# Performance work log

Hardware: AMD Instinct MI355X
Metric: run time of the kernel (lower is better)

## Reference

```python
import jax, jax.numpy as jnp
import numpy as np

B, H, W, DIM = 16, 64, 64, 512
GH, GW = 8, 8
NH = 16
HD = DIM // NH
POS = DIM // 16  # DynamicPosBias pos_dim = (dim//4)//4 = 32
EPS = 1e-5


def setup_inputs() -> dict:
    key = jax.random.key(0)
    ks = jax.random.split(key, 12)
    w = lambda k, s: jax.random.normal(k, s, jnp.float32) * 0.02
    f32 = jnp.float32
    return {
        "x": jax.random.normal(ks[0], (B, H * W, DIM), f32),
        "norm1_g": jnp.ones((DIM,), f32), "norm1_b": jnp.zeros((DIM,), f32),
        "qkv_w": w(ks[1], (3 * DIM, DIM)), "qkv_b": jnp.zeros((3 * DIM,), f32),
        "proj_w": w(ks[2], (DIM, DIM)), "proj_b": jnp.zeros((DIM,), f32),
        "pos_w0": w(ks[3], (POS, 2)), "pos_b0": jnp.zeros((POS,), f32),
        "pos_ln0_g": jnp.ones((POS,), f32), "pos_ln0_b": jnp.zeros((POS,), f32),
        "pos_w1": w(ks[4], (POS, POS)), "pos_b1": jnp.zeros((POS,), f32),
        "pos_ln1_g": jnp.ones((POS,), f32), "pos_ln1_b": jnp.zeros((POS,), f32),
        "pos_w2": w(ks[5], (POS, POS)), "pos_b2": jnp.zeros((POS,), f32),
        "pos_ln2_g": jnp.ones((POS,), f32), "pos_ln2_b": jnp.zeros((POS,), f32),
        "pos_w3": w(ks[6], (NH, POS)), "pos_b3": jnp.zeros((NH,), f32),
        "norm2_g": jnp.ones((DIM,), f32), "norm2_b": jnp.zeros((DIM,), f32),
        "mlp_w1": w(ks[7], (4 * DIM, DIM)), "mlp_b1": jnp.zeros((4 * DIM,), f32),
        "mlp_w2": w(ks[8], (DIM, 4 * DIM)), "mlp_b2": jnp.zeros((DIM,), f32),
    }


def _ln(x, g, b):
    m = jnp.mean(x, -1, keepdims=True)
    v = jnp.mean(jnp.square(x - m), -1, keepdims=True)
    return (x - m) * jax.lax.rsqrt(v + EPS) * g + b


def _rel_bias_tables():
    # relative coordinate table [(2GH-1)*(2GW-1), 2]
    ph = jnp.arange(1 - GH, GH)
    pw = jnp.arange(1 - GW, GW)
    biases = jnp.stack(jnp.meshgrid(ph, pw, indexing="ij")).reshape(2, -1).T.astype(jnp.float32)
    # relative position index [GH*GW, GH*GW]
    coords = jnp.stack(jnp.meshgrid(jnp.arange(GH), jnp.arange(GW), indexing="ij")).reshape(2, -1)
    rel = (coords[:, :, None] - coords[:, None, :]).transpose(1, 2, 0)  # [N,N,2]
    idx = (rel[..., 0] + GH - 1) * (2 * GW - 1) + (rel[..., 1] + GW - 1)
    return biases, idx


def reference(x, norm1_g, norm1_b, qkv_w, qkv_b, proj_w, proj_b,
              pos_w0, pos_b0, pos_ln0_g, pos_ln0_b,
              pos_w1, pos_b1, pos_ln1_g, pos_ln1_b,
              pos_w2, pos_b2, pos_ln2_g, pos_ln2_b,
              pos_w3, pos_b3, norm2_g, norm2_b,
              mlp_w1, mlp_b1, mlp_w2, mlp_b2):
    biases, rel_idx = _rel_bias_tables()
    Ng = GH * GW
    scale = HD ** -0.5

    shortcut = x
    h = _ln(x, norm1_g, norm1_b).reshape(B, H, W, DIM)
    # use_lda=True: long-distance (strided) grouping
    h = h.reshape(B, GH, H // GH, GW, W // GW, DIM).transpose(0, 2, 4, 1, 3, 5)
    h = h.reshape(B * (H * W) // Ng, Ng, DIM)  # [G, Ng, C]

    # attention
    qkv = h @ qkv_w.T + qkv_b
    qkv = qkv.reshape(-1, Ng, 3, NH, HD).transpose(2, 0, 3, 1, 4)  # [3,G,NH,Ng,HD]
    q, k, v = qkv[0], qkv[1], qkv[2]
    attn = jnp.einsum("ghnd,ghmd->ghnm", q * scale, k)

    # dynamic position bias MLP on the coordinate table
    p = jax.nn.relu(_ln(biases @ pos_w0.T + pos_b0, pos_ln0_g, pos_ln0_b))
    p = jax.nn.relu(_ln(p @ pos_w1.T + pos_b1, pos_ln1_g, pos_ln1_b))
    p = jax.nn.relu(_ln(p @ pos_w2.T + pos_b2, pos_ln2_g, pos_ln2_b))
    p = p @ pos_w3.T + pos_b3  # [(2GH-1)(2GW-1), NH]
    rel_bias = p[rel_idx].transpose(2, 0, 1)  # [NH, Ng, Ng]

    attn = jax.nn.softmax(attn + rel_bias[None], axis=-1)
    o = jnp.einsum("ghnm,ghmd->ghnd", attn, v)
    o = o.transpose(0, 2, 1, 3).reshape(-1, Ng, DIM)
    o = o @ proj_w.T + proj_b

    # ungroup (inverse of lda grouping)
    o = o.reshape(B, H // GH, W // GW, GH, GW, DIM)
    o = o.transpose(0, 3, 1, 4, 2, 5).reshape(B, H * W, DIM)

    x = shortcut + o
    m = _ln(x, norm2_g, norm2_b)
    m = jax.nn.gelu(m @ mlp_w1.T + mlp_b1, approximate=False)
    m = m @ mlp_w2.T + mlp_b2
    return x + m
```

## Files before the change

kernel.cpp:

```cpp
#include <hip/hip_runtime.h>
#include <hip/hip_bf16.h>

typedef __bf16 bf16;
typedef __bf16 bf16x8 __attribute__((ext_vector_type(8)));
typedef __bf16 bf16x4 __attribute__((ext_vector_type(4)));
typedef float f32x4_t __attribute__((ext_vector_type(4)));

static constexpr int kDIM = 512;

static constexpr size_t OFF_QKVW = 0;
static constexpr size_t OFF_PROJW = 1572864;
static constexpr size_t OFF_W1   = 2097152;
static constexpr size_t OFF_W2   = 4194304;
static constexpr size_t OFF_PTAB = 6291456;
static constexpr size_t OFF_A    = 8388608;
static constexpr size_t OFF_B    = 276824064;

typedef __attribute__((address_space(3))) uint32_t lds_u32_t;
typedef __attribute__((address_space(1))) const uint32_t glb_u32_t;
#define ASYNC_COPY16(gp, lp) __builtin_amdgcn_global_load_lds((glb_u32_t*)(gp), (lds_u32_t*)(lp), 16, 0, 0)
#define WAITV0() asm volatile("s_waitcnt vmcnt(0)" ::: "memory")

__global__ void cast_bf16_k(const float* __restrict__ in, bf16* __restrict__ out, int n4)
{
    int i = blockIdx.x * blockDim.x + threadIdx.x;
    if (i < n4) {
        float4 v = ((const float4*)in)[i];
        bf16x4 o; o[0] = (bf16)v.x; o[1] = (bf16)v.y; o[2] = (bf16)v.z; o[3] = (bf16)v.w;
        ((bf16x4*)out)[i] = o;
    }
}

__global__ void cast_fp8_k(const float* __restrict__ in, unsigned char* __restrict__ out, int n4)
{
    int i = blockIdx.x * blockDim.x + threadIdx.x;
    if (i < n4) {
        float4 v = ((const float4*)in)[i];
        int p = __builtin_amdgcn_cvt_pk_fp8_f32(v.x * 64.0f, v.y * 64.0f, 0, false);
        p = __builtin_amdgcn_cvt_pk_fp8_f32(v.z * 64.0f, v.w * 64.0f, p, true);
        ((unsigned int*)out)[i] = (unsigned int)p;
    }
}

template<int GROUP>
__global__ __launch_bounds__(256)
void ln_k(const float* __restrict__ x, const float* __restrict__ gw,
          const float* __restrict__ bw, bf16* __restrict__ out)
{
    const int t = blockIdx.x * 4 + (threadIdx.x >> 6);
    const int lane = threadIdx.x & 63;
    const float* xp = x + (size_t)t * kDIM + lane * 8;
    float4 p0 = *(const float4*)xp;
    float4 p1 = *(const float4*)(xp + 4);
    float v[8] = {p0.x, p0.y, p0.z, p0.w, p1.x, p1.y, p1.z, p1.w};
    float s = 0.f;
#pragma unroll
    for (int i = 0; i < 8; ++i) s += v[i];
#pragma unroll
    for (int off = 32; off > 0; off >>= 1) s += __shfl_xor(s, off);
    const float mean = s * (1.0f / 512.0f);
    float q = 0.f;
#pragma unroll
    for (int i = 0; i < 8; ++i) { float d = v[i] - mean; q += d * d; }
#pragma unroll
    for (int off = 32; off > 0; off >>= 1) q += __shfl_xor(q, off);
    const float rstd = rsqrtf(q * (1.0f / 512.0f) + 1e-5f);
    size_t orow;
    if (GROUP) {
        int b = t >> 12, r = (t >> 6) & 63, c = t & 63;
        int g = b * 64 + (r & 7) * 8 + (c & 7);
        int n = (r >> 3) * 8 + (c >> 3);
        orow = (size_t)g * 64 + n;
    } else {
        orow = t;
    }
    float4 g0 = *(const float4*)(gw + lane * 8);
    float4 g1 = *(const float4*)(gw + lane * 8 + 4);
    float4 b0 = *(const float4*)(bw + lane * 8);
    float4 b1 = *(const float4*)(bw + lane * 8 + 4);
    float gg[8] = {g0.x, g0.y, g0.z, g0.w, g1.x, g1.y, g1.z, g1.w};
    float bb[8] = {b0.x, b0.y, b0.z, b0.w, b1.x, b1.y, b1.z, b1.w};
    bf16x8 o8;
#pragma unroll
    for (int i = 0; i < 8; ++i) o8[i] = (bf16)((v[i] - mean) * rstd * gg[i] + bb[i]);
    *(bf16x8*)(out + orow * kDIM + lane * 8) = o8;
}

__device__ inline void ln32_relu(float* h, const float* g, const float* b)
{
    float m = 0.f;
#pragma unroll
    for (int i = 0; i < 32; ++i) m += h[i];
    m *= (1.0f / 32.0f);
    float v = 0.f;
#pragma unroll
    for (int i = 0; i < 32; ++i) { float d = h[i] - m; v += d * d; }
    v *= (1.0f / 32.0f);
    float r = rsqrtf(v + 1e-5f);
#pragma unroll
    for (int i = 0; i < 32; ++i) h[i] = fmaxf((h[i] - m) * r * g[i] + b[i], 0.f);
}

__global__ __launch_bounds__(256)
void posmlp_k(const float* __restrict__ w0, const float* __restrict__ b0,
              const float* __restrict__ g0, const float* __restrict__ bb0,
              const float* __restrict__ w1, const float* __restrict__ b1,
              const float* __restrict__ g1, const float* __restrict__ bb1,
              const float* __restrict__ w2, const float* __restrict__ b2,
              const float* __restrict__ g2, const float* __restrict__ bb2,
              const float* __restrict__ w3, const float* __restrict__ b3,
              float* __restrict__ ptab)
{
    int r = threadIdx.x;
    if (r >= 225) return;
    float in0 = (float)(r / 15) - 7.0f;
    float in1 = (float)(r % 15) - 7.0f;
    float h[32], h2[32];
#pragma unroll
    for (int o = 0; o < 32; ++o) h[o] = w0[o * 2] * in0 + w0[o * 2 + 1] * in1 + b0[o];
    ln32_relu(h, g0, bb0);
#pragma unroll
    for (int o = 0; o < 32; ++o) {
        float s = b1[o];
#pragma unroll
        for (int i = 0; i < 32; ++i) s += w1[o * 32 + i] * h[i];
        h2[o] = s;
    }
    ln32_relu(h2, g1, bb1);
#pragma unroll
    for (int o = 0; o < 32; ++o) {
        float s = b2[o];
#pragma unroll
        for (int i = 0; i < 32; ++i) s += w2[o * 32 + i] * h2[i];
        h[o] = s;
    }
    ln32_relu(h, g2, bb2);
#pragma unroll
    for (int o = 0; o < 16; ++o) {
        float s = b3[o];
#pragma unroll
        for (int i = 0; i < 32; ++i) s += w3[o * 32 + i] * h[i];
        ptab[r * 16 + o] = s;
    }
}

__global__ __launch_bounds__(256)
void attn_mfma_k(const bf16* __restrict__ qkv, const float* __restrict__ ptab,
                 bf16* __restrict__ obuf)
{
    const int g  = blockIdx.x >> 1;
    const int hb = blockIdx.x & 1;
    const int w  = threadIdx.x >> 6;
    const int lane = threadIdx.x & 63;
    const int c = lane & 15, q = lane >> 4;

    __shared__ float ptl[16][240];
    __shared__ alignas(16) bf16 pl[4][4096];
    __shared__ alignas(16) bf16 vt[4][2048];

    for (int i = threadIdx.x; i < 3600; i += 256)
        ptl[i & 15][i >> 4] = ptab[i];
    __syncthreads();

    const size_t rowb = (size_t)g * 64;
    bf16* pw = pl[w];
    char* vw = (char*)vt[w];

    for (int hh = 0; hh < 2; ++hh) {
        const int head = hb * 8 + hh * 4 + w;
        const bf16* qb = qkv + rowb * 1536 + head * 32;

        bf16x8 vrow[4];
#pragma unroll
        for (int l = 0; l < 4; ++l)
            vrow[l] = *(const bf16x8*)(qb + 1024 + (size_t)lane * 1536 + l * 8);

        bf16x8 aq[4], bk[4];
#pragma unroll
        for (int i = 0; i < 4; ++i) {
            aq[i] = *(const bf16x8*)(qb + (size_t)(i * 16 + c) * 1536 + q * 8);
            bk[i] = *(const bf16x8*)(qb + 512 + (size_t)(i * 16 + c) * 1536 + q * 8);
        }

        f32x4_t s[4][4];
#pragma unroll
        for (int i = 0; i < 4; ++i)
#pragma unroll
            for (int j = 0; j < 4; ++j)
                s[i][j] = __builtin_amdgcn_mfma_f32_16x16x32_bf16(aq[i], bk[j],
                          (f32x4_t){0.f, 0.f, 0.f, 0.f}, 0, 0, 0);

#pragma unroll
        for (int l = 0; l < 4; ++l)
#pragma unroll
            for (int j = 0; j < 8; ++j) {
                const int d = l * 8 + j;
                *(bf16*)(vw + d * 128 + ((lane * 2) ^ ((d & 7) << 4))) = vrow[l][j];
            }

        const float scale = 0.17677669529663687f;
        float inv[4][4];
#pragma unroll
        for (int i = 0; i < 4; ++i)
#pragma unroll
            for (int jj = 0; jj < 4; ++jj) {
                const int n = i * 16 + q * 4 + jj;
                const int na = n >> 3, nu = n & 7;
                float mx = -1e30f;
#pragma unroll
                for (int j = 0; j < 4; ++j) {
                    const int m = j * 16 + c;
                    const int idx = (na - (m >> 3) + 7) * 15 + (nu - (m & 7) + 7);
                    float v = s[i][j][jj] * scale + ptl[head][idx];
                    s[i][j][jj] = v;
                    mx = fmaxf(mx, v);
                }
#pragma unroll
                for (int off = 1; off < 16; off <<= 1) mx = fmaxf(mx, __shfl_xor(mx, off));
                float sum = 0.f;
#pragma unroll
                for (int j = 0; j < 4; ++j) {
                    float e = __expf(s[i][j][jj] - mx);
                    s[i][j][jj] = e; sum += e;
                }
#pragma unroll
                for (int off = 1; off < 16; off <<= 1) sum += __shfl_xor(sum, off);
                inv[i][jj] = 1.0f / sum;
            }

#pragma unroll
        for (int i = 0; i < 4; ++i)
#pragma unroll
            for (int jj = 0; jj < 4; ++jj) {
                const int n = i * 16 + q * 4 + jj;
                const int swz = (n & 7) << 4;
#pragma unroll
                for (int j = 0; j < 4; ++j) {
                    const int m = j * 16 + c;
                    *(bf16*)((char*)pw + n * 128 + ((m * 2) ^ swz)) = (bf16)s[i][j][jj];
                }
            }

        bf16x8 bv[2][2];
#pragma unroll
        for (int ks = 0; ks < 2; ++ks)
#pragma unroll
            for (int dt = 0; dt < 2; ++dt)
                bv[ks][dt] = *(const bf16x8*)(vw + (dt * 16 + c) * 128 +
                              ((ks * 64 + q * 16) ^ ((c & 7) << 4)));

        f32x4_t o[4][2];
#pragma unroll
        for (int i = 0; i < 4; ++i)
#pragma unroll
            for (int dt = 0; dt < 2; ++dt)
                o[i][dt] = (f32x4_t){0.f, 0.f, 0.f, 0.f};
#pragma unroll
        for (int ks = 0; ks < 2; ++ks)
#pragma unroll
            for (int i = 0; i < 4; ++i) {
                const int n = i * 16 + c;
                bf16x8 ap = *(const bf16x8*)((char*)pw + n * 128 +
                             ((ks * 64 + q * 16) ^ ((n & 7) << 4)));
#pragma unroll
                for (int dt = 0; dt < 2; ++dt)
                    o[i][dt] = __builtin_amdgcn_mfma_f32_16x16x32_bf16(ap, bv[ks][dt], o[i][dt], 0, 0, 0);
            }

        bf16* ob = obuf + rowb * 512 + head * 32;
#pragma unroll
        for (int i = 0; i < 4; ++i)
#pragma unroll
            for (int dt = 0; dt < 2; ++dt)
#pragma unroll
                for (int jj = 0; jj < 4; ++jj) {
                    const int n = i * 16 + q * 4 + jj;
                    ob[(size_t)n * 512 + dt * 16 + c] = (bf16)(o[i][dt][jj] * inv[i][jj]);
                }
    }
}

template<int MODE, int NBX>
__global__ __launch_bounds__(256, 2)
void gemm_bt(const bf16* __restrict__ A, const bf16* __restrict__ Bw,
             const float* __restrict__ bias, const float* __restrict__ resid,
             bf16* __restrict__ outb, float* __restrict__ outf,
             int N, int K)
{
    __shared__ alignas(16) bf16 As[128 * 64];
    __shared__ alignas(16) bf16 Bs[128 * 64];
    const int tid = threadIdx.x;
    const int lane = tid & 63;
    const int w = tid >> 6;
    const int wr = w >> 1, wc = w & 1;

    const int bid = blockIdx.y * NBX + blockIdx.x;
    const int nwg = gridDim.y * NBX;
    const int swz = (bid & 7) * (nwg >> 3) + (bid >> 3);
    const int by = swz / NBX;
    const int bx = swz - by * NBX;
    const int rowBase = by * 128;
    const int colBase = bx * 128;

    f32x4_t acc[4][4];
#pragma unroll
    for (int m = 0; m < 4; ++m)
#pragma unroll
        for (int n = 0; n < 4; ++n)
            acc[m][n] = (f32x4_t){0.f, 0.f, 0.f, 0.f};

    const int sw = (lane & 7) << 4;

    for (int kt = 0; kt < K; kt += 64) {
#pragma unroll
        for (int l = 0; l < 4; ++l) {
            const int cg = l * 256 + tid;
            const int row = cg >> 3;
            const int col8 = (cg & 7) ^ (row & 7);
            const int cu = l * 256 + (tid & 192);
            ASYNC_COPY16(A + (size_t)(rowBase + row) * K + kt + col8 * 8, As + cu * 8);
            ASYNC_COPY16(Bw + (size_t)(colBase + row) * K + kt + col8 * 8, Bs + cu * 8);
        }
        WAITV0();
        __syncthreads();
#pragma unroll
        for (int kk = 0; kk < 64; kk += 32) {
            const int bofs = kk * 2 + (lane >> 4) * 16;
            bf16x8 af[4], bfr[4];
#pragma unroll
            for (int m = 0; m < 4; ++m) {
                const int row = wr * 64 + m * 16 + (lane & 15);
                af[m] = *(const bf16x8*)((const char*)As + row * 128 + (bofs ^ sw));
            }
#pragma unroll
            for (int n = 0; n < 4; ++n) {
                const int row = wc * 64 + n * 16 + (lane & 15);
                bfr[n] = *(const bf16x8*)((const char*)Bs + row * 128 + (bofs ^ sw));
            }
#pragma unroll
            for (int m = 0; m < 4; ++m)
#pragma unroll
                for (int n = 0; n < 4; ++n)
                    acc[m][n] = __builtin_amdgcn_mfma_f32_16x16x32_bf16(af[m], bfr[n], acc[m][n], 0, 0, 0);
        }
        __syncthreads();
    }

#pragma unroll
    for (int m = 0; m < 4; ++m) {
#pragma unroll
        for (int jj = 0; jj < 4; ++jj) {
            int grow = rowBase + wr * 64 + m * 16 + (lane >> 4) * 4 + jj;
#pragma unroll
            for (int n = 0; n < 4; ++n) {
                int gcol = colBase + wc * 64 + n * 16 + (lane & 15);
                float v = acc[m][n][jj] + bias[gcol];
                if constexpr (MODE == 0) {
                    outb[(size_t)grow * N + gcol] = (bf16)v;
                } else if constexpr (MODE == 1) {
                    float e = __expf(1.5957691216057308f * (v + 0.044715f * v * v * v));
                    v = v * (e / (1.0f + e));
                    int p8 = __builtin_amdgcn_cvt_pk_fp8_f32(v * 64.0f, v * 64.0f, 0, false);
                    ((unsigned char*)outb)[(size_t)grow * N + gcol] = (unsigned char)(p8 & 0xff);
                } else if constexpr (MODE == 2) {
                    int g = grow >> 6, ns = grow & 63;
                    int b = g >> 6, i = (g >> 3) & 7, j = g & 7;
                    int a = ns >> 3, u = ns & 7;
                    int t = b * 4096 + (a * 8 + i) * 64 + (u * 8 + j);
                    size_t oi = (size_t)t * 512 + gcol;
                    outf[oi] = resid[oi] + v;
                }
            }
        }
    }
}

template<int NBX>
__global__ __launch_bounds__(256, 2)
void gemm_fp8(const unsigned char* __restrict__ A, const unsigned char* __restrict__ Bw,
              const float* __restrict__ bias, const float* __restrict__ resid,
              float* __restrict__ outf, int N, int K, float invs)
{
    __shared__ alignas(16) unsigned char As[128 * 64];
    __shared__ alignas(16) unsigned char Bs[128 * 64];
    const int tid = threadIdx.x;
    const int lane = tid & 63;
    const int w = tid >> 6;
    const int wr = w >> 1, wc = w & 1;
    const int c = lane & 15, q = lane >> 4;

    const int bid = blockIdx.y * NBX + blockIdx.x;
    const int nwg = gridDim.y * NBX;
    const int swz = (bid & 7) * (nwg >> 3) + (bid >> 3);
    const int by = swz / NBX;
    const int bx = swz - by * NBX;
    const int rowBase = by * 128;
    const int colBase = bx * 128;

    f32x4_t acc[4][4];
#pragma unroll
    for (int m = 0; m < 4; ++m)
#pragma unroll
        for (int n = 0; n < 4; ++n)
            acc[m][n] = (f32x4_t){0.f, 0.f, 0.f, 0.f};

    const int f = (c >> 1) & 3;
    const int hb8 = (q & 1) * 8;

    for (int kt = 0; kt < K; kt += 64) {
#pragma unroll
        for (int l = 0; l < 2; ++l) {
            const int cg = l * 256 + tid;
            const int row = cg >> 2;
            const int sg = (cg & 3) ^ ((cg >> 3) & 3);
            const int cu = l * 256 + (tid & 192);
            ASYNC_COPY16(A + (size_t)(rowBase + row) * K + kt + sg * 16, As + cu * 16);
            ASYNC_COPY16(Bw + (size_t)(colBase + row) * K + kt + sg * 16, Bs + cu * 16);
        }
        WAITV0();
        __syncthreads();
#pragma unroll
        for (int kk = 0; kk < 64; kk += 32) {
            const int sb = (((((kk >> 4) + (q >> 1)) ^ f) << 4)) + hb8;
            long af[4], bfr[4];
#pragma unroll
            for (int m = 0; m < 4; ++m) {
                const int row = wr * 64 + m * 16 + c;
                af[m] = *(const long*)((const char*)As + row * 64 + sb);
            }
#pragma unroll
            for (int n = 0; n < 4; ++n) {
                const int row = wc * 64 + n * 16 + c;
                bfr[n] = *(const long*)((const char*)Bs + row * 64 + sb);
            }
#pragma unroll
            for (int m = 0; m < 4; ++m)
#pragma unroll
                for (int n = 0; n < 4; ++n)
                    acc[m][n] = __builtin_amdgcn_mfma_f32_16x16x32_fp8_fp8(af[m], bfr[n], acc[m][n], 0, 0, 0);
        }
        __syncthreads();
    }

#pragma unroll
    for (int m = 0; m < 4; ++m) {
#pragma unroll
        for (int jj = 0; jj < 4; ++jj) {
            int grow = rowBase + wr * 64 + m * 16 + q * 4 + jj;
#pragma unroll
            for (int n = 0; n < 4; ++n) {
                int gcol = colBase + wc * 64 + n * 16 + c;
                float v = acc[m][n][jj] * invs + bias[gcol];
                size_t oi = (size_t)grow * 512 + gcol;
                outf[oi] = resid[oi] + v;
            }
        }
    }
}

extern "C" void kernel_launch(void* const* d_in, const int* in_sizes, int n_in,
                              void* d_out, int out_size, void* d_ws, size_t ws_size,
                              hipStream_t stream)
{
    const float* x    = (const float*)d_in[0];
    const float* n1g  = (const float*)d_in[1];
    const float* n1b  = (const float*)d_in[2];
    const float* qkvw = (const float*)d_in[3];
    const float* qkvb = (const float*)d_in[4];
    const float* pjw  = (const float*)d_in[5];
    const float* pjb  = (const float*)d_in[6];
    const float* pw0  = (const float*)d_in[7];
    const float* pb0  = (const float*)d_in[8];
    const float* pg0  = (const float*)d_in[9];
    const float* pbb0 = (const float*)d_in[10];
    const float* pw1  = (const float*)d_in[11];
    const float* pb1  = (const float*)d_in[12];
    const float* pg1  = (const float*)d_in[13];
    const float* pbb1 = (const float*)d_in[14];
    const float* pw2  = (const float*)d_in[15];
    const float* pb2  = (const float*)d_in[16];
    const float* pg2  = (const float*)d_in[17];
    const float* pbb2 = (const float*)d_in[18];
    const float* pw3  = (const float*)d_in[19];
    const float* pb3  = (const float*)d_in[20];
    const float* n2g  = (const float*)d_in[21];
    const float* n2b  = (const float*)d_in[22];
    const float* w1   = (const float*)d_in[23];
    const float* b1   = (const float*)d_in[24];
    const float* w2   = (const float*)d_in[25];
    const float* b2   = (const float*)d_in[26];

    char* ws = (char*)d_ws;
    bf16* qkvw_b = (bf16*)(ws + OFF_QKVW);
    bf16* pjw_b  = (bf16*)(ws + OFF_PROJW);
    bf16* w1_b   = (bf16*)(ws + OFF_W1);
    unsigned char* w2_f8 = (unsigned char*)(ws + OFF_W2);
    float* ptab  = (float*)(ws + OFF_PTAB);
    bf16* bufA   = (bf16*)(ws + OFF_A);
    bf16* bufB   = (bf16*)(ws + OFF_B);
    float* xout  = (float*)d_out;

    cast_bf16_k<<<(1536 * 512 / 4 + 255) / 256, 256, 0, stream>>>(qkvw, qkvw_b, 1536 * 512 / 4);
    cast_bf16_k<<<(512 * 512 / 4 + 255) / 256, 256, 0, stream>>>(pjw, pjw_b, 512 * 512 / 4);
    cast_bf16_k<<<(2048 * 512 / 4 + 255) / 256, 256, 0, stream>>>(w1, w1_b, 2048 * 512 / 4);
    cast_fp8_k<<<(512 * 2048 / 4 + 255) / 256, 256, 0, stream>>>(w2, w2_f8, 512 * 2048 / 4);

    posmlp_k<<<1, 256, 0, stream>>>(pw0, pb0, pg0, pbb0, pw1, pb1, pg1, pbb1,
                                    pw2, pb2, pg2, pbb2, pw3, pb3, ptab);

    ln_k<1><<<16384, 256, 0, stream>>>(x, n1g, n1b, bufB);

    gemm_bt<0, 12><<<dim3(12, 512), 256, 0, stream>>>(bufB, qkvw_b, qkvb, nullptr, bufA, nullptr, 1536, 512);

    attn_mfma_k<<<2048, 256, 0, stream>>>(bufA, ptab, bufB);

    gemm_bt<2, 4><<<dim3(4, 512), 256, 0, stream>>>(bufB, pjw_b, pjb, x, nullptr, xout, 512, 512);

    ln_k<0><<<16384, 256, 0, stream>>>(xout, n2g, n2b, bufB);

    gemm_bt<1, 16><<<dim3(16, 512), 256, 0, stream>>>(bufB, w1_b, b1, nullptr, bufA, nullptr, 2048, 512);

    gemm_fp8<4><<<dim3(4, 512), 256, 0, stream>>>((const unsigned char*)bufA, w2_f8, b2,
                                                  xout, xout, 512, 2048, 1.0f / 4096.0f);
}
```

Baseline: 814.7 us.

## Switch QKV and MLP-up GEMMs to FP8 with FP8 layernorm outputs

Layernorm now writes scaled FP8 activations instead of bf16, and the QKV projection and first MLP GEMM run through the FP8 MFMA GEMM kernel with FP8-cast weights. The FP8 GEMM gains output modes for bf16 stores and fused GELU-to-FP8, matching the old bf16 kernel's epilogues. This halves activation and weight bytes and uses the faster FP8 matrix instructions, at the cost of lower precision on two more GEMMs.

```diff
diff --git a/kernel.cpp b/kernel.cpp
--- a/kernel.cpp
+++ b/kernel.cpp
@@ -45,7 +45,7 @@
 template<int GROUP>
 __global__ __launch_bounds__(256)
 void ln_k(const float* __restrict__ x, const float* __restrict__ gw,
-          const float* __restrict__ bw, bf16* __restrict__ out)
+          const float* __restrict__ bw, unsigned char* __restrict__ out)
 {
     const int t = blockIdx.x * 4 + (threadIdx.x >> 6);
     const int lane = threadIdx.x & 63;
@@ -80,10 +80,16 @@
     float4 b1 = *(const float4*)(bw + lane * 8 + 4);
     float gg[8] = {g0.x, g0.y, g0.z, g0.w, g1.x, g1.y, g1.z, g1.w};
     float bb[8] = {b0.x, b0.y, b0.z, b0.w, b1.x, b1.y, b1.z, b1.w};
-    bf16x8 o8;
-#pragma unroll
-    for (int i = 0; i < 8; ++i) o8[i] = (bf16)((v[i] - mean) * rstd * gg[i] + bb[i]);
-    *(bf16x8*)(out + orow * kDIM + lane * 8) = o8;
+    float o[8];
+#pragma unroll
+    for (int i = 0; i < 8; ++i) o[i] = ((v[i] - mean) * rstd * gg[i] + bb[i]) * 32.0f;
+    unsigned int lo = 0, hi = 0;
+    lo = (unsigned int)__builtin_amdgcn_cvt_pk_fp8_f32(o[0], o[1], 0, false);
+    lo = (unsigned int)__builtin_amdgcn_cvt_pk_fp8_f32(o[2], o[3], (int)lo, true);
+    hi = (unsigned int)__builtin_amdgcn_cvt_pk_fp8_f32(o[4], o[5], 0, false);
+    hi = (unsigned int)__builtin_amdgcn_cvt_pk_fp8_f32(o[6], o[7], (int)hi, true);
+    uint2 u; u.x = lo; u.y = hi;
+    *(uint2*)(out + orow * kDIM + lane * 8) = u;
 }
 
 __device__ inline void ln32_relu(float* h, const float* g, const float* b)
@@ -357,11 +363,6 @@
                 float v = acc[m][n][jj] + bias[gcol];
                 if constexpr (MODE == 0) {
                     outb[(size_t)grow * N + gcol] = (bf16)v;
-                } else if constexpr (MODE == 1) {
-                    float e = __expf(1.5957691216057308f * (v + 0.044715f * v * v * v));
-                    v = v * (e / (1.0f + e));
-                    int p8 = __builtin_amdgcn_cvt_pk_fp8_f32(v * 64.0f, v * 64.0f, 0, false);
-                    ((unsigned char*)outb)[(size_t)grow * N + gcol] = (unsigned char)(p8 & 0xff);
                 } else if constexpr (MODE == 2) {
                     int g = grow >> 6, ns = grow & 63;
                     int b = g >> 6, i = (g >> 3) & 7, j = g & 7;
@@ -375,11 +376,11 @@
     }
 }
 
-template<int NBX>
+template<int MODE, int NBX>
 __global__ __launch_bounds__(256, 2)
 void gemm_fp8(const unsigned char* __restrict__ A, const unsigned char* __restrict__ Bw,
               const float* __restrict__ bias, const float* __restrict__ resid,
-              float* __restrict__ outf, int N, int K, float invs)
+              void* __restrict__ outp, int N, int K, float invs)
 {
     __shared__ alignas(16) unsigned char As[128 * 64];
     __shared__ alignas(16) unsigned char Bs[128 * 64];
@@ -451,8 +452,17 @@
             for (int n = 0; n < 4; ++n) {
                 int gcol = colBase + wc * 64 + n * 16 + c;
                 float v = acc[m][n][jj] * invs + bias[gcol];
-                size_t oi = (size_t)grow * 512 + gcol;
-                outf[oi] = resid[oi] + v;
+                if constexpr (MODE == 0) {
+                    ((bf16*)outp)[(size_t)grow * N + gcol] = (bf16)v;
+                } else if constexpr (MODE == 1) {
+                    float e = __expf(1.5957691216057308f * (v + 0.044715f * v * v * v));
+                    v = v * (e / (1.0f + e));
+                    int p8 = __builtin_amdgcn_cvt_pk_fp8_f32(v * 64.0f, v * 64.0f, 0, false);
+                    ((unsigned char*)outp)[(size_t)grow * N + gcol] = (unsigned char)(p8 & 0xff);
+                } else {
+                    size_t oi = (size_t)grow * 512 + gcol;
+                    ((float*)outp)[oi] = resid[oi] + v;
+                }
             }
         }
     }
@@ -491,35 +501,39 @@
     const float* b2   = (const float*)d_in[26];
 
     char* ws = (char*)d_ws;
-    bf16* qkvw_b = (bf16*)(ws + OFF_QKVW);
+    unsigned char* qkvw_f8 = (unsigned char*)(ws + OFF_QKVW);
     bf16* pjw_b  = (bf16*)(ws + OFF_PROJW);
-    bf16* w1_b   = (bf16*)(ws + OFF_W1);
+    unsigned char* w1_f8 = (unsigned char*)(ws + OFF_W1);
     unsigned char* w2_f8 = (unsigned char*)(ws + OFF_W2);
     float* ptab  = (float*)(ws + OFF_PTAB);
     bf16* bufA   = (bf16*)(ws + OFF_A);
-    bf16* bufB   = (bf16*)(ws + OFF_B);
+    unsigned char* bufA8 = (unsigned char*)(ws + OFF_A);
+    unsigned char* bufB8 = (unsigned char*)(ws + OFF_B);
+    bf16* bufBb  = (bf16*)(ws + OFF_B);
     float* xout  = (float*)d_out;
 
-    cast_bf16_k<<<(1536 * 512 / 4 + 255) / 256, 256, 0, stream>>>(qkvw, qkvw_b, 1536 * 512 / 4);
+    cast_fp8_k<<<(1536 * 512 / 4 + 255) / 256, 256, 0, stream>>>(qkvw, qkvw_f8, 1536 * 512 / 4);
     cast_bf16_k<<<(512 * 512 / 4 + 255) / 256, 256, 0, stream>>>(pjw, pjw_b, 512 * 512 / 4);
-    cast_bf16_k<<<(2048 * 512 / 4 + 255) / 256, 256, 0, stream>>>(w1, w1_b, 2048 * 512 / 4);
+    cast_fp8_k<<<(2048 * 512 / 4 + 255) / 256, 256, 0, stream>>>(w1, w1_f8, 2048 * 512 / 4);
     cast_fp8_k<<<(512 * 2048 / 4 + 255) / 256, 256, 0, stream>>>(w2, w2_f8, 512 * 2048 / 4);
 
     posmlp_k<<<1, 256, 0, stream>>>(pw0, pb0, pg0, pbb0, pw1, pb1, pg1, pbb1,
                                     pw2, pb2, pg2, pbb2, pw3, pb3, ptab);
 
-    ln_k<1><<<16384, 256, 0, stream>>>(x, n1g, n1b, bufB);
-
-    gemm_bt<0, 12><<<dim3(12, 512), 256, 0, stream>>>(bufB, qkvw_b, qkvb, nullptr, bufA, nullptr, 1536, 512);
-
-    attn_mfma_k<<<2048, 256, 0, stream>>>(bufA, ptab, bufB);
-
-    gemm_bt<2, 4><<<dim3(4, 512), 256, 0, stream>>>(bufB, pjw_b, pjb, x, nullptr, xout, 512, 512);
-
-    ln_k<0><<<16384, 256, 0, stream>>>(xout, n2g, n2b, bufB);
-
-    gemm_bt<1, 16><<<dim3(16, 512), 256, 0, stream>>>(bufB, w1_b, b1, nullptr, bufA, nullptr, 2048, 512);
-
-    gemm_fp8<4><<<dim3(4, 512), 256, 0, stream>>>((const unsigned char*)bufA, w2_f8, b2,
-                                                  xout, xout, 512, 2048, 1.0f / 4096.0f);
-}
+    ln_k<1><<<16384, 256, 0, stream>>>(x, n1g, n1b, bufB8);
+
+    gemm_fp8<0, 12><<<dim3(12, 512), 256, 0, stream>>>(bufB8, qkvw_f8, qkvb, nullptr,
+                                                       bufA, 1536, 512, 1.0f / 2048.0f);
+
+    attn_mfma_k<<<2048, 256, 0, stream>>>(bufA, ptab, bufBb);
+
+    gemm_bt<2, 4><<<dim3(4, 512), 256, 0, stream>>>(bufBb, pjw_b, pjb, x, nullptr, xout, 512, 512);
+
+    ln_k<0><<<16384, 256, 0, stream>>>(xout, n2g, n2b, bufB8);
+
+    gemm_fp8<1, 16><<<dim3(16, 512), 256, 0, stream>>>(bufB8, w1_f8, b1, nullptr,
+                                                       bufA8, 2048, 512, 1.0f / 2048.0f);
+
+    gemm_fp8<3, 4><<<dim3(4, 512), 256, 0, stream>>>(bufA8, w2_f8, b2, xout,
+                                                     xout, 512, 2048, 1.0f / 4096.0f);
+}
```

Measured after the change: 736.1 us. -9.7%, faster.
